# Performance work log

Measured on AMD Instinct MI355X. Metric: run time of the kernel, lower is better.

## Reference

```python
import jax, jax.numpy as jnp
import numpy as np

NEG_POS_RATIO = 3
B, P, C = 128, 8732, 21  # batch, SSD300 priors, VOC classes (hardcoded 21 in original)


def setup_inputs() -> dict:
    key = jax.random.key(0)
    k1, k2, k3, k4, k5, k6 = jax.random.split(key, 6)
    confidence = jax.random.normal(k1, (B, P, C), jnp.float32)
    predicted_locations = jax.random.normal(k2, (B, P, 4), jnp.float32)
    gt_locations = jax.random.normal(k3, (B, P, 4), jnp.float32)
    raw_labels = jax.random.randint(k4, (B, P), 0, C)
    keep = jax.random.uniform(k5, (B, P)) < 0.03
    labels = jnp.where(keep, raw_labels, 0).astype(jnp.int64)
    mask = jax.random.uniform(k6, (B, P), jnp.float32)
    return {
        "confidence": confidence,
        "predicted_locations": predicted_locations,
        "labels": labels,
        "gt_locations": gt_locations,
        "mask": mask,
    }


def _hard_negative_mining(bg_loss, labels, neg_pos_ratio):
    # Faithful to SSD box_utils.hard_negative_mining.
    pos_mask = labels > 0                                   # [B,P] bool
    num_pos = pos_mask.sum(axis=1, keepdims=True)           # [B,1]
    num_neg = num_pos * neg_pos_ratio                       # [B,1]
    masked = jnp.where(pos_mask, -jnp.inf, bg_loss)         # positives excluded
    idx = jnp.argsort(-masked, axis=1)                      # descending by loss
    orders = jnp.argsort(idx, axis=1)                       # rank of each prior
    neg_mask = orders < num_neg                             # top num_neg hardest
    return pos_mask, neg_mask


def reference(confidence, predicted_locations, labels, gt_locations, mask):
    nls = -jax.nn.log_softmax(confidence, axis=-1)          # [B,P,C]
    bg_loss = nls[:, :, 0]                                  # [B,P]
    pos_mask, neg_mask = _hard_negative_mining(bg_loss, labels, NEG_POS_RATIO)
    posf = pos_mask.astype(nls.dtype)

    # per-prior NLL at the assigned label, weighted by mask over positives
    per_label = jnp.take_along_axis(nls, labels[..., None], axis=2)[..., 0]  # [B,P]
    confidence_pos_loss = (mask * per_label * posf).sum()
    confidence_neg_loss = jnp.where(neg_mask, bg_loss, 0.0).sum()
    confidence_loss = confidence_pos_loss + confidence_neg_loss

    # smooth-L1 over positive priors, weighted by mask (broadcast over 4 coords)
    d = predicted_locations - gt_locations                  # [B,P,4]
    ad = jnp.abs(d)
    sl1 = jnp.where(ad < 1.0, 0.5 * d * d, ad - 0.5)
    regression_loss = (sl1 * (mask * posf)[..., None]).sum()

    all_batch_pos = mask.sum()
    return regression_loss / all_batch_pos, confidence_loss / all_batch_pos
```

## Files before the change

kernel.cpp:

```cpp
#include <hip/hip_runtime.h>
#include <stdint.h>

#define BATCH 128
#define PRI   8732
#define NCLS  21
#define NPR   3
#define TOTAL (BATCH * PRI)
#define NBLK  (TOTAL / 256)
#define NPART (TOTAL / 64)


typedef const __attribute__((address_space(1))) void gv_t;
typedef __attribute__((address_space(3))) void lv_t;

__global__ __launch_bounds__(256)
void k_main(const float* __restrict__ conf, const float* __restrict__ pred,
            const int* __restrict__ labels, const float* __restrict__ gt,
            const float* __restrict__ mask, uint32_t* __restrict__ keys,
            float* __restrict__ pm, float* __restrict__ pp, float* __restrict__ pr)
{
  __shared__ __align__(16) float sconf[256 * NCLS];
  const int tid = threadIdx.x;
  const int wv  = tid >> 6;
  const int ln  = tid & 63;
  const long long wbase = ((long long)blockIdx.x * 4 + wv) * 64;

  const float4* src4  = (const float4*)(conf + wbase * NCLS);
  float*        slice = sconf + wv * (64 * NCLS);

  #pragma unroll
  for (int i = 0; i < 5; ++i) {
    __builtin_amdgcn_global_load_lds(
        (gv_t*)(src4 + i * 64 + ln),
        (lv_t*)((float4*)slice + i * 64),
        16, 0, 0);
  }
  if (ln < 16) {
    __builtin_amdgcn_global_load_lds(
        (gv_t*)(src4 + 320 + ln),
        (lv_t*)((float4*)slice + 320),
        16, 0, 0);
  }

  const long long a = wbase + ln;
  const int   lab = labels[a];
  const float mk  = mask[a];

  asm volatile("s_waitcnt vmcnt(0)" ::: "memory");

  const float* cv = &slice[ln * NCLS];
  float m = cv[0];
  #pragma unroll
  for (int c = 1; c < NCLS; ++c) m = fmaxf(m, cv[c]);
  float s = 0.f;
  #pragma unroll
  for (int c = 0; c < NCLS; ++c) s += __expf(cv[c] - m);
  const float lse = m + __logf(s);
  const float bg  = lse - cv[0];
  const bool  pos = lab > 0;

  float accm = mk, accp = 0.f, accr = 0.f;
  if (pos) {
    accp = mk * (lse - cv[lab]);
    const float4 pd = ((const float4*)pred)[a];
    const float4 g  = ((const float4*)gt)[a];
    float sl = 0.f, d, ad;
    d = pd.x - g.x; ad = fabsf(d); sl += (ad < 1.f) ? 0.5f * d * d : ad - 0.5f;
    d = pd.y - g.y; ad = fabsf(d); sl += (ad < 1.f) ? 0.5f * d * d : ad - 0.5f;
    d = pd.z - g.z; ad = fabsf(d); sl += (ad < 1.f) ? 0.5f * d * d : ad - 0.5f;
    d = pd.w - g.w; ad = fabsf(d); sl += (ad < 1.f) ? 0.5f * d * d : ad - 0.5f;
    accr = mk * sl;
  }
  keys[a] = pos ? 0u : (__float_as_uint(bg) | 0x80000000u);

  #pragma unroll
  for (int o = 32; o > 0; o >>= 1) {
    accm += __shfl_down(accm, o);
    accp += __shfl_down(accp, o);
    accr += __shfl_down(accr, o);
  }
  if (ln == 0) {
    const int gw = blockIdx.x * 4 + wv;
    pm[gw] = accm; pp[gw] = accp; pr[gw] = accr;
  }
}

#define SEL_T 512
#define RPT   18

__global__ __launch_bounds__(SEL_T)
void k_select(const uint32_t* __restrict__ keys, double* __restrict__ neg)
{
  __shared__ int    slots[16 * 24 + 8];
  __shared__ int    ired[8];
  __shared__ double dred[8];
  const int tid  = threadIdx.x;
  const int w    = tid >> 6;
  const int lane = tid & 63;
  const uint32_t* row = keys + (size_t)blockIdx.x * PRI;

  uint32_t kr[RPT];
  #pragma unroll
  for (int r = 0; r < 17; ++r) kr[r] = row[tid + 512 * r];
  kr[17] = (tid < 28) ? row[tid + 8704] : 0u;

  int zc = 0;
  #pragma unroll
  for (int r = 0; r < 17; ++r) zc += (kr[r] == 0u) ? 1 : 0;
  if (tid < 28) zc += (kr[17] == 0u) ? 1 : 0;
  #pragma unroll
  for (int o = 32; o > 0; o >>= 1) zc += __shfl_down(zc, o);
  if (lane == 0) ired[w] = zc;
  __syncthreads();
  int np = 0;
  #pragma unroll
  for (int i = 0; i < 8; ++i) np += ired[i];

  int k = np * NPR;
  const int nneg = PRI - np;
  if (k > nneg) k = nneg;

  double result = 0.0;
  if (k > 0) {
    uint32_t cur = 0x80000000u;
    #pragma unroll 1
    for (int bit = 30; bit >= 1; bit -= 2) {
      const int rnd = (30 - bit) >> 1;
      const uint32_t tA = cur | (3u << (bit - 1));
      const uint32_t tB = cur | (1u << bit);
      const uint32_t tC = cur | (1u << (bit - 1));
      int cA = 0, cB = 0, cC = 0;
      #pragma unroll
      for (int r = 0; r < RPT; ++r) {
        cA += (int)__popcll(__ballot(kr[r] >= tA));
        cB += (int)__popcll(__ballot(kr[r] >= tB));
        cC += (int)__popcll(__ballot(kr[r] >= tC));
      }
      if (lane == 0) {
        int* sl = &slots[rnd * 24];
        sl[w] = cA; sl[8 + w] = cB; sl[16 + w] = cC;
      }
      __syncthreads();
      int TA = 0, TB = 0, TC = 0;
      const int* sl = &slots[rnd * 24];
      #pragma unroll
      for (int i = 0; i < 8; ++i) { TA += sl[i]; TB += sl[8 + i]; TC += sl[16 + i]; }
      cur = (TA >= k) ? tA : (TB >= k) ? tB : (TC >= k) ? tC : cur;
    }
    {
      const uint32_t t = cur | 1u;
      int c = 0;
      #pragma unroll
      for (int r = 0; r < RPT; ++r) c += (int)__popcll(__ballot(kr[r] >= t));
      if (lane == 0) slots[16 * 24 + w] = c;
      __syncthreads();
      int tot = 0;
      #pragma unroll
      for (int i = 0; i < 8; ++i) tot += slots[16 * 24 + i];
      if (tot >= k) cur = t;
    }

    const float thr = __uint_as_float(cur & 0x7fffffffu);
    double ssum = 0.0;
    int g = 0;
    #pragma unroll
    for (int r = 0; r < RPT; ++r) {
      if (kr[r] > cur) { ssum += (double)__uint_as_float(kr[r] & 0x7fffffffu); ++g; }
    }
    #pragma unroll
    for (int o = 32; o > 0; o >>= 1) { ssum += __shfl_down(ssum, o); g += __shfl_down(g, o); }
    if (lane == 0) { dred[w] = ssum; ired[w] = g; }
    __syncthreads();
    if (tid == 0) {
      double tot = 0.0; int gg = 0;
      #pragma unroll
      for (int i = 0; i < 8; ++i) { tot += dred[i]; gg += ired[i]; }
      result = tot + (double)(k - gg) * (double)thr;
    }
  }
  if (tid == 0) neg[blockIdx.x] = result;
}

__global__ __launch_bounds__(256)
void k_final(const float* __restrict__ pm, const float* __restrict__ pp,
             const float* __restrict__ pr, const double* __restrict__ neg,
             float* __restrict__ out)
{
  __shared__ double red[4][4];
  const int tid = threadIdx.x, w = tid >> 6, lane = tid & 63;
  double sm = 0.0, sp = 0.0, sr = 0.0, sn = 0.0;
  for (int i = tid; i < NPART; i += 256) {
    sm += (double)pm[i]; sp += (double)pp[i]; sr += (double)pr[i];
  }
  if (tid < BATCH) sn = neg[tid];
  #pragma unroll
  for (int o = 32; o > 0; o >>= 1) {
    sm += __shfl_down(sm, o); sp += __shfl_down(sp, o);
    sr += __shfl_down(sr, o); sn += __shfl_down(sn, o);
  }
  if (lane == 0) { red[0][w] = sm; red[1][w] = sp; red[2][w] = sr; red[3][w] = sn; }
  __syncthreads();
  if (tid == 0) {
    double m = 0, p = 0, r = 0, n = 0;
    #pragma unroll
    for (int i = 0; i < 4; ++i) { m += red[0][i]; p += red[1][i]; r += red[2][i]; n += red[3][i]; }
    out[0] = (float)(r / m);
    out[1] = (float)((p + n) / m);
  }
}

extern "C" void kernel_launch(void* const* d_in, const int* in_sizes, int n_in,
                              void* d_out, int out_size, void* d_ws, size_t ws_size,
                              hipStream_t stream) {
  const float* conf   = (const float*)d_in[0];
  const float* pred   = (const float*)d_in[1];
  const int*   labels = (const int*)d_in[2];
  const float* gt     = (const float*)d_in[3];
  const float* mask   = (const float*)d_in[4];
  float* out = (float*)d_out;

  char* ws = (char*)d_ws;
  const size_t keys_bytes = (size_t)TOTAL * sizeof(uint32_t);
  uint32_t* keys = (uint32_t*)ws;
  float*  pm  = (float*)(ws + keys_bytes);
  float*  pp  = pm + NPART;
  float*  pr  = pp + NPART;
  double* neg = (double*)(ws + keys_bytes + (size_t)3 * NPART * sizeof(float));

  k_main<<<NBLK, 256, 0, stream>>>(conf, pred, labels, gt, mask, keys, pm, pp, pr);
  k_select<<<BATCH, SEL_T, 0, stream>>>(keys, neg);
  k_final<<<1, 256, 0, stream>>>(pm, pp, pr, neg, out);
}
```

Baseline: 207.7 us.

## Replace LDS staging with register double-buffered loads over multiple chunks per block

The main kernel drops the global-to-LDS async copy of the confidence rows. Each thread now loads its 21 logits straight into registers with unaligned vector loads. Each block handles up to four 256-prior chunks and prefetches the next chunk while computing the current one. The pred/gt loads and the label gather become unconditional and branch-free, so every prior reads location data and not just positives, which adds memory traffic. Per-thread strided row loads of 84 bytes are less coalesced than the old LDS staging, and the double-buffered registers raise register pressure.

Result: no change. 204.3 us (-1.7%).

```diff
diff --git a/kernel.cpp b/kernel.cpp
--- a/kernel.cpp
+++ b/kernel.cpp
@@ -1,17 +1,44 @@
 #include <hip/hip_runtime.h>
 #include <stdint.h>
 
-#define BATCH 128
-#define PRI   8732
-#define NCLS  21
-#define NPR   3
-#define TOTAL (BATCH * PRI)
-#define NBLK  (TOTAL / 256)
-#define NPART (TOTAL / 64)
-
-
-typedef const __attribute__((address_space(1))) void gv_t;
-typedef __attribute__((address_space(3))) void lv_t;
+#define BATCH  128
+#define PRI    8732
+#define NCLS   21
+#define NPR    3
+#define TOTAL  (BATCH * PRI)
+#define NCHUNK (TOTAL / 256)
+#define CPBLK  4
+#define GBLK   1092
+#define NPART  (GBLK * 4)
+
+
+typedef float f4a4 __attribute__((ext_vector_type(4), aligned(4)));
+
+struct Pf {
+  f4a4  q0, q1, q2, q3, q4;
+  float t;
+  int   lab;
+  float mk;
+  float4 pd, g;
+};
+
+__device__ __forceinline__ void issue(Pf& p, const float* __restrict__ conf,
+                                      const float* __restrict__ pred,
+                                      const float* __restrict__ gt,
+                                      const int* __restrict__ labels,
+                                      const float* __restrict__ mask, long long a) {
+  const float* ap = conf + a * NCLS;
+  p.q0 = *(const f4a4*)(ap);
+  p.q1 = *(const f4a4*)(ap + 4);
+  p.q2 = *(const f4a4*)(ap + 8);
+  p.q3 = *(const f4a4*)(ap + 12);
+  p.q4 = *(const f4a4*)(ap + 16);
+  p.t  = ap[20];
+  p.lab = labels[a];
+  p.mk  = mask[a];
+  p.pd  = ((const float4*)pred)[a];
+  p.g   = ((const float4*)gt)[a];
+}
 
 __global__ __launch_bounds__(256)
 void k_main(const float* __restrict__ conf, const float* __restrict__ pred,
@@ -19,59 +46,58 @@
             const float* __restrict__ mask, uint32_t* __restrict__ keys,
             float* __restrict__ pm, float* __restrict__ pp, float* __restrict__ pr)
 {
-  __shared__ __align__(16) float sconf[256 * NCLS];
   const int tid = threadIdx.x;
-  const int wv  = tid >> 6;
-  const int ln  = tid & 63;
-  const long long wbase = ((long long)blockIdx.x * 4 + wv) * 64;
-
-  const float4* src4  = (const float4*)(conf + wbase * NCLS);
-  float*        slice = sconf + wv * (64 * NCLS);
-
-  #pragma unroll
-  for (int i = 0; i < 5; ++i) {
-    __builtin_amdgcn_global_load_lds(
-        (gv_t*)(src4 + i * 64 + ln),
-        (lv_t*)((float4*)slice + i * 64),
-        16, 0, 0);
-  }
-  if (ln < 16) {
-    __builtin_amdgcn_global_load_lds(
-        (gv_t*)(src4 + 320 + ln),
-        (lv_t*)((float4*)slice + 320),
-        16, 0, 0);
-  }
-
-  const long long a = wbase + ln;
-  const int   lab = labels[a];
-  const float mk  = mask[a];
-
-  asm volatile("s_waitcnt vmcnt(0)" ::: "memory");
-
-  const float* cv = &slice[ln * NCLS];
-  float m = cv[0];
-  #pragma unroll
-  for (int c = 1; c < NCLS; ++c) m = fmaxf(m, cv[c]);
-  float s = 0.f;
-  #pragma unroll
-  for (int c = 0; c < NCLS; ++c) s += __expf(cv[c] - m);
-  const float lse = m + __logf(s);
-  const float bg  = lse - cv[0];
-  const bool  pos = lab > 0;
-
-  float accm = mk, accp = 0.f, accr = 0.f;
-  if (pos) {
-    accp = mk * (lse - cv[lab]);
-    const float4 pd = ((const float4*)pred)[a];
-    const float4 g  = ((const float4*)gt)[a];
+  const int b   = blockIdx.x;
+  int nch = NCHUNK - b * CPBLK;
+  if (nch <= 0) return;
+  if (nch > CPBLK) nch = CPBLK;
+
+  long long ca = (long long)b * (CPBLK * 256) + tid;
+
+  Pf pf;
+  issue(pf, conf, pred, gt, labels, mask, ca);
+
+  float accm = 0.f, accp = 0.f, accr = 0.f;
+
+  #pragma unroll 1
+  for (int it = 0; it < nch; ++it) {
+    Pf cur = pf;
+    const long long a = ca;
+    if (it + 1 < nch) {
+      ca += 256;
+      issue(pf, conf, pred, gt, labels, mask, ca);
+    }
+
+    float c[21] = { cur.q0.x, cur.q0.y, cur.q0.z, cur.q0.w,
+                    cur.q1.x, cur.q1.y, cur.q1.z, cur.q1.w,
+                    cur.q2.x, cur.q2.y, cur.q2.z, cur.q2.w,
+                    cur.q3.x, cur.q3.y, cur.q3.z, cur.q3.w,
+                    cur.q4.x, cur.q4.y, cur.q4.z, cur.q4.w, cur.t };
+    float m = c[0];
+    #pragma unroll
+    for (int i = 1; i < NCLS; ++i) m = fmaxf(m, c[i]);
+    float s = 0.f, sel = c[0];
+    #pragma unroll
+    for (int i = 0; i < NCLS; ++i) {
+      s += __expf(c[i] - m);
+      if (i > 0) sel = (cur.lab == i) ? c[i] : sel;
+    }
+    const float lse = m + __logf(s);
+    const float bg  = lse - c[0];
+    const bool  pos = cur.lab > 0;
+
     float sl = 0.f, d, ad;
-    d = pd.x - g.x; ad = fabsf(d); sl += (ad < 1.f) ? 0.5f * d * d : ad - 0.5f;
-    d = pd.y - g.y; ad = fabsf(d); sl += (ad < 1.f) ? 0.5f * d * d : ad - 0.5f;
-    d = pd.z - g.z; ad = fabsf(d); sl += (ad < 1.f) ? 0.5f * d * d : ad - 0.5f;
-    d = pd.w - g.w; ad = fabsf(d); sl += (ad < 1.f) ? 0.5f * d * d : ad - 0.5f;
-    accr = mk * sl;
-  }
-  keys[a] = pos ? 0u : (__float_as_uint(bg) | 0x80000000u);
+    d = cur.pd.x - cur.g.x; ad = fabsf(d); sl += (ad < 1.f) ? 0.5f * d * d : ad - 0.5f;
+    d = cur.pd.y - cur.g.y; ad = fabsf(d); sl += (ad < 1.f) ? 0.5f * d * d : ad - 0.5f;
+    d = cur.pd.z - cur.g.z; ad = fabsf(d); sl += (ad < 1.f) ? 0.5f * d * d : ad - 0.5f;
+    d = cur.pd.w - cur.g.w; ad = fabsf(d); sl += (ad < 1.f) ? 0.5f * d * d : ad - 0.5f;
+    const float w = pos ? cur.mk : 0.f;
+    accm += cur.mk;
+    accp += w * (lse - sel);
+    accr += w * sl;
+
+    keys[a] = pos ? 0u : (__float_as_uint(bg) | 0x80000000u);
+  }
 
   #pragma unroll
   for (int o = 32; o > 0; o >>= 1) {
@@ -79,8 +105,8 @@
     accp += __shfl_down(accp, o);
     accr += __shfl_down(accr, o);
   }
-  if (ln == 0) {
-    const int gw = blockIdx.x * 4 + wv;
+  if ((tid & 63) == 0) {
+    const int gw = b * 4 + (tid >> 6);
     pm[gw] = accm; pp[gw] = accp; pr[gw] = accr;
   }
 }
@@ -227,7 +253,7 @@
   float*  pr  = pp + NPART;
   double* neg = (double*)(ws + keys_bytes + (size_t)3 * NPART * sizeof(float));
 
-  k_main<<<NBLK, 256, 0, stream>>>(conf, pred, labels, gt, mask, keys, pm, pp, pr);
+  k_main<<<GBLK, 256, 0, stream>>>(conf, pred, labels, gt, mask, keys, pm, pp, pr);
   k_select<<<BATCH, SEL_T, 0, stream>>>(keys, neg);
   k_final<<<1, 256, 0, stream>>>(pm, pp, pr, neg, out);
 }
```

## Process four 64-prior chunks per wave with register prefetch of next chunk

Applied to the files above, without the earlier changes.

Each wave now handles 256 priors in four sequential chunks instead of 64. It prefetches the next chunk's confidence, labels, mask and locations into registers while computing the current one, and replaces the direct global-to-LDS loads with register loads followed by LDS stores. The label gather and the smooth-L1 branch become branch-free selects. The intent is to overlap memory latency with compute and cut the block count, at the cost of fewer waves for latency hiding, higher register pressure, and reading pred/gt for all priors instead of only positives.

Result: slower. 246.5 us (+18.6%).

```diff
diff --git a/kernel.cpp b/kernel.cpp
--- a/kernel.cpp
+++ b/kernel.cpp
@@ -1,17 +1,14 @@
 #include <hip/hip_runtime.h>
 #include <stdint.h>
 
-#define BATCH 128
-#define PRI   8732
-#define NCLS  21
-#define NPR   3
-#define TOTAL (BATCH * PRI)
-#define NBLK  (TOTAL / 256)
-#define NPART (TOTAL / 64)
-
-
-typedef const __attribute__((address_space(1))) void gv_t;
-typedef __attribute__((address_space(3))) void lv_t;
+#define BATCH  128
+#define PRI    8732
+#define NCLS   21
+#define NPR    3
+#define TOTAL  (BATCH * PRI)
+#define NWAVE  (TOTAL / 256)
+#define GBLK   ((NWAVE + 3) / 4)
+
 
 __global__ __launch_bounds__(256)
 void k_main(const float* __restrict__ conf, const float* __restrict__ pred,
@@ -19,59 +16,92 @@
             const float* __restrict__ mask, uint32_t* __restrict__ keys,
             float* __restrict__ pm, float* __restrict__ pp, float* __restrict__ pr)
 {
-  __shared__ __align__(16) float sconf[256 * NCLS];
+  __shared__ __align__(16) float scratch[4 * 64 * NCLS];
   const int tid = threadIdx.x;
   const int wv  = tid >> 6;
   const int ln  = tid & 63;
-  const long long wbase = ((long long)blockIdx.x * 4 + wv) * 64;
-
-  const float4* src4  = (const float4*)(conf + wbase * NCLS);
-  float*        slice = sconf + wv * (64 * NCLS);
-
-  #pragma unroll
-  for (int i = 0; i < 5; ++i) {
-    __builtin_amdgcn_global_load_lds(
-        (gv_t*)(src4 + i * 64 + ln),
-        (lv_t*)((float4*)slice + i * 64),
-        16, 0, 0);
-  }
-  if (ln < 16) {
-    __builtin_amdgcn_global_load_lds(
-        (gv_t*)(src4 + 320 + ln),
-        (lv_t*)((float4*)slice + 320),
-        16, 0, 0);
-  }
-
-  const long long a = wbase + ln;
-  const int   lab = labels[a];
-  const float mk  = mask[a];
-
-  asm volatile("s_waitcnt vmcnt(0)" ::: "memory");
-
-  const float* cv = &slice[ln * NCLS];
-  float m = cv[0];
-  #pragma unroll
-  for (int c = 1; c < NCLS; ++c) m = fmaxf(m, cv[c]);
-  float s = 0.f;
-  #pragma unroll
-  for (int c = 0; c < NCLS; ++c) s += __expf(cv[c] - m);
-  const float lse = m + __logf(s);
-  const float bg  = lse - cv[0];
-  const bool  pos = lab > 0;
-
-  float accm = mk, accp = 0.f, accr = 0.f;
-  if (pos) {
-    accp = mk * (lse - cv[lab]);
-    const float4 pd = ((const float4*)pred)[a];
-    const float4 g  = ((const float4*)gt)[a];
-    float sl = 0.f, d, ad;
-    d = pd.x - g.x; ad = fabsf(d); sl += (ad < 1.f) ? 0.5f * d * d : ad - 0.5f;
-    d = pd.y - g.y; ad = fabsf(d); sl += (ad < 1.f) ? 0.5f * d * d : ad - 0.5f;
-    d = pd.z - g.z; ad = fabsf(d); sl += (ad < 1.f) ? 0.5f * d * d : ad - 0.5f;
-    d = pd.w - g.w; ad = fabsf(d); sl += (ad < 1.f) ? 0.5f * d * d : ad - 0.5f;
-    accr = mk * sl;
-  }
-  keys[a] = pos ? 0u : (__float_as_uint(bg) | 0x80000000u);
+  const int gw  = blockIdx.x * 4 + wv;
+  if (gw >= NWAVE) return;
+
+  float*  sl  = scratch + wv * (64 * NCLS);
+  float4* sl4 = (float4*)sl;
+  const long long base0 = (long long)gw * 256;
+
+  float4 qa[5], qta, pda, ga;
+  int laba; float mka;
+  {
+    const float4* s4 = (const float4*)(conf + base0 * NCLS);
+    #pragma unroll
+    for (int j = 0; j < 5; ++j) qa[j] = s4[j * 64 + ln];
+    qta = (ln < 16) ? s4[320 + ln] : make_float4(0.f, 0.f, 0.f, 0.f);
+    laba = labels[base0 + ln];
+    mka  = mask[base0 + ln];
+    pda  = ((const float4*)pred)[base0 + ln];
+    ga   = ((const float4*)gt)[base0 + ln];
+  }
+
+  float accm = 0.f, accp = 0.f, accr = 0.f;
+
+  #pragma unroll 1
+  for (int c = 0; c < 4; ++c) {
+    const long long a0 = base0 + c * 64;
+    const long long a  = a0 + ln;
+
+    float4 q[5], qt, pd, g;
+    #pragma unroll
+    for (int j = 0; j < 5; ++j) q[j] = qa[j];
+    qt = qta; pd = pda; g = ga;
+    const int   lab = laba;
+    const float mk  = mka;
+
+    if (c + 1 < 4) {
+      const long long n0 = a0 + 64;
+      const float4* s4 = (const float4*)(conf + n0 * NCLS);
+      #pragma unroll
+      for (int j = 0; j < 5; ++j) qa[j] = s4[j * 64 + ln];
+      if (ln < 16) qta = s4[320 + ln];
+      laba = labels[n0 + ln];
+      mka  = mask[n0 + ln];
+      pda  = ((const float4*)pred)[n0 + ln];
+      ga   = ((const float4*)gt)[n0 + ln];
+    }
+
+    __builtin_amdgcn_wave_barrier();
+    #pragma unroll
+    for (int j = 0; j < 5; ++j) sl4[j * 64 + ln] = q[j];
+    if (ln < 16) sl4[320 + ln] = qt;
+    __builtin_amdgcn_wave_barrier();
+
+    const float* cp = sl + ln * NCLS;
+    float cv[NCLS];
+    #pragma unroll
+    for (int i = 0; i < NCLS; ++i) cv[i] = cp[i];
+
+    float m = cv[0];
+    #pragma unroll
+    for (int i = 1; i < NCLS; ++i) m = fmaxf(m, cv[i]);
+    float s = 0.f, selv = cv[0];
+    #pragma unroll
+    for (int i = 0; i < NCLS; ++i) {
+      s += __expf(cv[i] - m);
+      if (i > 0) selv = (lab == i) ? cv[i] : selv;
+    }
+    const float lse = m + __logf(s);
+    const float bg  = lse - cv[0];
+    const bool  pos = lab > 0;
+
+    float slr = 0.f, d, ad;
+    d = pd.x - g.x; ad = fabsf(d); slr += (ad < 1.f) ? 0.5f * d * d : ad - 0.5f;
+    d = pd.y - g.y; ad = fabsf(d); slr += (ad < 1.f) ? 0.5f * d * d : ad - 0.5f;
+    d = pd.z - g.z; ad = fabsf(d); slr += (ad < 1.f) ? 0.5f * d * d : ad - 0.5f;
+    d = pd.w - g.w; ad = fabsf(d); slr += (ad < 1.f) ? 0.5f * d * d : ad - 0.5f;
+    const float w = pos ? mk : 0.f;
+    accm += mk;
+    accp += w * (lse - selv);
+    accr += w * slr;
+
+    keys[a] = pos ? 0u : (__float_as_uint(bg) | 0x80000000u);
+  }
 
   #pragma unroll
   for (int o = 32; o > 0; o >>= 1) {
@@ -79,10 +109,7 @@
     accp += __shfl_down(accp, o);
     accr += __shfl_down(accr, o);
   }
-  if (ln == 0) {
-    const int gw = blockIdx.x * 4 + wv;
-    pm[gw] = accm; pp[gw] = accp; pr[gw] = accr;
-  }
+  if (ln == 0) { pm[gw] = accm; pp[gw] = accp; pr[gw] = accr; }
 }
 
 #define SEL_T 512
@@ -189,7 +216,7 @@
   __shared__ double red[4][4];
   const int tid = threadIdx.x, w = tid >> 6, lane = tid & 63;
   double sm = 0.0, sp = 0.0, sr = 0.0, sn = 0.0;
-  for (int i = tid; i < NPART; i += 256) {
+  for (int i = tid; i < NWAVE; i += 256) {
     sm += (double)pm[i]; sp += (double)pp[i]; sr += (double)pr[i];
   }
   if (tid < BATCH) sn = neg[tid];
@@ -223,11 +250,12 @@
   const size_t keys_bytes = (size_t)TOTAL * sizeof(uint32_t);
   uint32_t* keys = (uint32_t*)ws;
   float*  pm  = (float*)(ws + keys_bytes);
-  float*  pp  = pm + NPART;
-  float*  pr  = pp + NPART;
-  double* neg = (double*)(ws + keys_bytes + (size_t)3 * NPART * sizeof(float));
-
-  k_main<<<NBLK, 256, 0, stream>>>(conf, pred, labels, gt, mask, keys, pm, pp, pr);
+  float*  pp  = pm + NWAVE;
+  float*  pr  = pp + NWAVE;
+  double* neg = (double*)(ws + keys_bytes +
+                          (((size_t)3 * NWAVE * sizeof(float) + 7) & ~(size_t)7));
+
+  k_main<<<GBLK, 256, 0, stream>>>(conf, pred, labels, gt, mask, keys, pm, pp, pr);
   k_select<<<BATCH, SEL_T, 0, stream>>>(keys, neg);
   k_final<<<1, 256, 0, stream>>>(pm, pp, pr, neg, out);
 }
```
